# Optimization experiments

Measured on AMD Instinct MI355X. Metric: run time of the kernel, lower is better.

The kernel has to match this reference:

```python
import jax, jax.numpy as jnp
import numpy as np

N_NODES = 50000
N_EDGES = 800000
NODE_DIM = 256
EDGE_DIM = 64
HIDDEN = 256
LN_EPS = 1e-5


def setup_inputs() -> dict:
    key = jax.random.key(0)
    ks = jax.random.split(key, 12)
    s = 0.05
    return {
        "edge_attr": jax.random.normal(ks[0], (N_EDGES, EDGE_DIM), jnp.float32),
        "node_attr": jax.random.normal(ks[1], (N_NODES, NODE_DIM), jnp.float32),
        "edge_index": jax.random.randint(ks[2], (2, N_EDGES), 0, N_NODES, jnp.int64),
        # split first linear: [hidden, edge_dim], [hidden, node_dim], [hidden, node_dim]
        "edge_lin": jax.random.normal(ks[3], (HIDDEN, EDGE_DIM), jnp.float32) * s,
        "src_lin": jax.random.normal(ks[4], (HIDDEN, NODE_DIM), jnp.float32) * s,
        "dst_lin": jax.random.normal(ks[5], (HIDDEN, NODE_DIM), jnp.float32) * s,
        "bias": jax.random.normal(ks[6], (HIDDEN,), jnp.float32) * s,
        # mlp: ReLU -> Linear(hidden,hidden) -> ReLU -> Linear(hidden,edge_dim) -> LayerNorm
        "W1": jax.random.normal(ks[7], (HIDDEN, HIDDEN), jnp.float32) * s,
        "b1": jax.random.normal(ks[8], (HIDDEN,), jnp.float32) * s,
        "W2": jax.random.normal(ks[9], (EDGE_DIM, HIDDEN), jnp.float32) * s,
        "b2": jax.random.normal(ks[10], (EDGE_DIM,), jnp.float32) * s,
        "ln_gamma": jnp.ones((EDGE_DIM,), jnp.float32),
        "ln_beta": jnp.zeros((EDGE_DIM,), jnp.float32),
    }


def reference(edge_attr, node_attr, edge_index, edge_lin, src_lin, dst_lin,
              bias, W1, b1, W2, b2, ln_gamma, ln_beta):
    # pre-project nodes once, then gather per-edge (sum trick)
    mlp_edge = edge_attr @ edge_lin.T                 # [E, H]
    mlp_src = node_attr @ src_lin.T                   # [N, H]
    mlp_dst = node_attr @ dst_lin.T + bias            # [N, H]
    src, dst = edge_index[0], edge_index[1]
    h = mlp_edge + mlp_src[src] + mlp_dst[dst]        # [E, H]
    # MLP: ReLU -> Linear -> ReLU -> Linear -> LayerNorm
    h = jax.nn.relu(h)
    h = jax.nn.relu(h @ W1.T + b1)                    # [E, H]
    y = h @ W2.T + b2                                 # [E, edge_dim]
    mu = jnp.mean(y, axis=-1, keepdims=True)
    var = jnp.mean(jnp.square(y - mu), axis=-1, keepdims=True)
    y = (y - mu) * jax.lax.rsqrt(var + LN_EPS) * ln_gamma + ln_beta
    return y
```

## Files before the change

kernel.cpp:

```cpp
#include <hip/hip_runtime.h>
#include <stdint.h>

#define EN 800000
#define NN 50000
#define HID 256
#define ED 64
#define LN_EPS 1e-5f

typedef __attribute__((ext_vector_type(8))) short bf8_t;
typedef __attribute__((ext_vector_type(4))) float f32x4;

union BF8 { unsigned short u[8]; bf8_t v; };

__device__ __forceinline__ unsigned short f2bf(float f) {
  union { float f; uint32_t u; } x; x.f = f;
  return (unsigned short)((x.u + 0x7FFFu + ((x.u >> 16) & 1u)) >> 16);
}
__device__ __forceinline__ float bf2f(uint32_t h) {
  union { uint32_t u; float f; } x; x.u = h << 16;
  return x.f;
}
__device__ __forceinline__ bf8_t pack8(float4 f0, float4 f1) {
  BF8 u;
  u.u[0] = f2bf(f0.x); u.u[1] = f2bf(f0.y); u.u[2] = f2bf(f0.z); u.u[3] = f2bf(f0.w);
  u.u[4] = f2bf(f1.x); u.u[5] = f2bf(f1.y); u.u[6] = f2bf(f1.z); u.u[7] = f2bf(f1.w);
  return u.v;
}

#define MFMA(a, b, c) __builtin_amdgcn_mfma_f32_16x16x32_bf16((a), (b), (c), 0, 0, 0)

__device__ __forceinline__ void gl_lds16(const void* g, void* l) {
  __builtin_amdgcn_global_load_lds(
      (const __attribute__((address_space(1))) void*)g,
      (__attribute__((address_space(3))) void*)l, 16, 0, 0);
}

__global__ void k_cvt_w(const float* __restrict__ W1, const float* __restrict__ W2,
                        const float* __restrict__ EL,
                        unsigned short* __restrict__ W1b, unsigned short* __restrict__ W2b,
                        unsigned short* __restrict__ ELb) {
  int i = blockIdx.x * blockDim.x + threadIdx.x;
  int stride = blockDim.x * gridDim.x;
  for (int j = i; j < HID * HID; j += stride) W1b[j] = f2bf(W1[j]);
  for (int j = i; j < ED * HID; j += stride) W2b[j] = f2bf(W2[j]);
  for (int j = i; j < HID * ED; j += stride) ELb[j] = f2bf(EL[j]);
}

__launch_bounds__(256)
__global__ void k_node_proj(const float* __restrict__ node_attr,
                            const float* __restrict__ src_lin,
                            const float* __restrict__ dst_lin,
                            const float* __restrict__ bias,
                            unsigned short* __restrict__ Psrc,
                            unsigned short* __restrict__ Pdst) {
  __shared__ __align__(16) char s_a[64 * 512];
  const int tid = threadIdx.x;
  const int wid = tid >> 6;
  const int lane = tid & 63;
  const int l16 = lane & 15, lq = lane >> 4;
  const int m0 = blockIdx.x * 64;

  for (int c = tid; c < 64 * 32; c += 256) {
    int row = c >> 5, kc = c & 31;
    int grow = m0 + row;
    bf8_t val;
    if (grow < NN) {
      const float4* p = (const float4*)(node_attr + (size_t)grow * HID + kc * 8);
      val = pack8(p[0], p[1]);
    } else {
      BF8 z;
      #pragma unroll
      for (int j = 0; j < 8; ++j) z.u[j] = 0;
      val = z.v;
    }
    *(bf8_t*)(s_a + row * 512 + ((kc ^ (row & 7)) << 4)) = val;
  }
  __syncthreads();

  const int n0 = wid * 64;
  for (int pass = 0; pass < 2; ++pass) {
    const float* W = pass ? dst_lin : src_lin;
    f32x4 acc[4][4] = {};
    #pragma unroll
    for (int ks = 0; ks < 8; ++ks) {
      bf8_t a[4], b[4];
      #pragma unroll
      for (int mi = 0; mi < 4; ++mi) {
        int row = mi * 16 + l16;
        a[mi] = *(const bf8_t*)(s_a + row * 512 + (((ks * 4 + lq) ^ (row & 7)) << 4));
      }
      #pragma unroll
      for (int ni = 0; ni < 4; ++ni) {
        const float4* p = (const float4*)(W + (size_t)(n0 + ni * 16 + l16) * HID + ks * 32 + lq * 8);
        b[ni] = pack8(p[0], p[1]);
      }
      #pragma unroll
      for (int mi = 0; mi < 4; ++mi)
        #pragma unroll
        for (int ni = 0; ni < 4; ++ni)
          acc[mi][ni] = MFMA(a[mi], b[ni], acc[mi][ni]);
    }
    unsigned short* P = pass ? Pdst : Psrc;
    #pragma unroll
    for (int ni = 0; ni < 4; ++ni) {
      int col = n0 + ni * 16 + l16;
      float bia = pass ? bias[col] : 0.f;
      #pragma unroll
      for (int mi = 0; mi < 4; ++mi) {
        #pragma unroll
        for (int r = 0; r < 4; ++r) {
          int row = m0 + mi * 16 + lq * 4 + r;
          if (row < NN) P[(size_t)row * HID + col] = f2bf(acc[mi][ni][r] + bia);
        }
      }
    }
  }
}

__launch_bounds__(256, 3)
__global__ void k_gather_g1(const float* __restrict__ edge_attr,
                            const int* __restrict__ edge_index,
                            const unsigned short* __restrict__ Psrc,
                            const unsigned short* __restrict__ Pdst,
                            const unsigned short* __restrict__ ELb,
                            unsigned short* __restrict__ H0,
                            int chunk_base) {
  __shared__ __align__(16) char s_h[64 * 512];
  __shared__ __align__(16) char s_e[64 * 128];
  __shared__ int s_src[64], s_dst[64];

  const int tid = threadIdx.x;
  const int wid = tid >> 6;
  const int lane = tid & 63;
  const int l16 = lane & 15, lq = lane >> 4;
  const int e0 = chunk_base + blockIdx.x * 64;
  const int h0 = blockIdx.x * 64;
  const int n0 = wid * 64;

  if (tid < 64) s_src[tid] = edge_index[e0 + tid];
  else if (tid < 128) s_dst[tid - 64] = edge_index[EN + e0 + (tid - 64)];

  #pragma unroll
  for (int i = 0; i < 2; ++i) {
    int c = tid + i * 256;
    int row = c >> 3, kc = c & 7;
    const float4* p = (const float4*)(edge_attr + (size_t)(e0 + row) * ED + kc * 8);
    *(bf8_t*)(s_e + row * 128 + ((kc ^ (row & 7)) << 4)) = pack8(p[0], p[1]);
  }
  __syncthreads();

  #pragma unroll 4
  for (int i = 0; i < 16; ++i) {
    int er = wid * 16 + i;
    int s = s_src[er], d = s_dst[er];
    const uint2* ps = (const uint2*)(Psrc + (size_t)s * HID) + lane;
    const uint2* pd = (const uint2*)(Pdst + (size_t)d * HID) + lane;
    uint2 a = *ps, b = *pd;
    float v0 = bf2f(a.x & 0xffffu) + bf2f(b.x & 0xffffu);
    float v1 = bf2f(a.x >> 16)     + bf2f(b.x >> 16);
    float v2 = bf2f(a.y & 0xffffu) + bf2f(b.y & 0xffffu);
    float v3 = bf2f(a.y >> 16)     + bf2f(b.y >> 16);
    uint2 o;
    o.x = (uint32_t)f2bf(v0) | ((uint32_t)f2bf(v1) << 16);
    o.y = (uint32_t)f2bf(v2) | ((uint32_t)f2bf(v3) << 16);
    int chunk = lane >> 1;
    *(uint2*)(s_h + er * 512 + ((chunk ^ (er & 7)) << 4) + ((lane & 1) << 3)) = o;
  }

  f32x4 acc[4][4] = {};
  #pragma unroll
  for (int ks = 0; ks < 2; ++ks) {
    bf8_t a[4], b[4];
    #pragma unroll
    for (int mi = 0; mi < 4; ++mi) {
      int row = mi * 16 + l16;
      a[mi] = *(const bf8_t*)(s_e + row * 128 + (((ks * 4 + lq) ^ (row & 7)) << 4));
    }
    #pragma unroll
    for (int ni = 0; ni < 4; ++ni)
      b[ni] = *(const bf8_t*)(ELb + (n0 + ni * 16 + l16) * ED + ks * 32 + lq * 8);
    #pragma unroll
    for (int mi = 0; mi < 4; ++mi)
      #pragma unroll
      for (int ni = 0; ni < 4; ++ni)
        acc[mi][ni] = MFMA(a[mi], b[ni], acc[mi][ni]);
  }
  __syncthreads();

  #pragma unroll
  for (int mi = 0; mi < 4; ++mi) {
    #pragma unroll
    for (int ni = 0; ni < 4; ++ni) {
      int col = n0 + ni * 16 + l16;
      #pragma unroll
      for (int r = 0; r < 4; ++r) {
        int row = mi * 16 + lq * 4 + r;
        unsigned short* p = (unsigned short*)(s_h + row * 512 +
                              (((col >> 3) ^ (row & 7)) << 4) + ((col & 7) << 1));
        float v = acc[mi][ni][r] + bf2f(*p);
        *p = f2bf(fmaxf(v, 0.f));
      }
    }
  }
  __syncthreads();

  #pragma unroll
  for (int i = 0; i < 8; ++i) {
    int c = tid + i * 256;
    int row = c >> 5, kc = c & 31;
    bf8_t val = *(const bf8_t*)(s_h + row * 512 + ((kc ^ (row & 7)) << 4));
    *(bf8_t*)(H0 + ((size_t)(h0 + row) << 8) + kc * 8) = val;
  }
}

__launch_bounds__(256, 2)
__global__ void k_mlp(const unsigned short* __restrict__ H0,
                      const unsigned short* __restrict__ W1b,
                      const unsigned short* __restrict__ W2b,
                      const float* __restrict__ b1,
                      const float* __restrict__ b2,
                      const float* __restrict__ gam,
                      const float* __restrict__ bet,
                      float* __restrict__ out,
                      int chunk_base) {
  __shared__ __align__(16) char s_a[64 * 512];
  __shared__ __align__(16) char s_b[256 * 128];

  const int tid = threadIdx.x;
  const int wid = tid >> 6;
  const int lane = tid & 63;
  const int l16 = lane & 15, lq = lane >> 4;
  const int eloc = blockIdx.x * 64;
  const int eglob = chunk_base + eloc;
  const int n0 = wid * 64;

  #pragma unroll
  for (int i = 0; i < 8; ++i) {
    int c = wid * 8 + i;
    int row = 2 * c + (lane >> 5);
    int srcc = (lane & 31) ^ (row & 7);
    gl_lds16(H0 + ((size_t)(eloc + row) << 8) + srcc * 8, s_a + c * 1024);
  }

  f32x4 acc[4][4] = {};
  for (int ks = 0; ks < 4; ++ks) {
    if (ks) __syncthreads();
    #pragma unroll
    for (int i = 0; i < 8; ++i) {
      int c = wid * 8 + i;
      int rown = 8 * c + (lane >> 3);
      int srcc = (lane & 7) ^ (rown & 7);
      gl_lds16(W1b + (size_t)rown * HID + ks * 64 + srcc * 8, s_b + c * 1024);
    }
    __syncthreads();

    #pragma unroll
    for (int ks2 = 0; ks2 < 2; ++ks2) {
      bf8_t a[4], b[4];
      #pragma unroll
      for (int mi = 0; mi < 4; ++mi) {
        int row = mi * 16 + l16;
        int c16 = ks * 8 + ks2 * 4 + lq;
        a[mi] = *(const bf8_t*)(s_a + row * 512 + ((c16 ^ (row & 7)) << 4));
      }
      #pragma unroll
      for (int ni = 0; ni < 4; ++ni) {
        int row = n0 + ni * 16 + l16;
        int c16 = ks2 * 4 + lq;
        b[ni] = *(const bf8_t*)(s_b + row * 128 + ((c16 ^ (row & 7)) << 4));
      }
      #pragma unroll
      for (int mi = 0; mi < 4; ++mi)
        #pragma unroll
        for (int ni = 0; ni < 4; ++ni)
          acc[mi][ni] = MFMA(a[mi], b[ni], acc[mi][ni]);
    }
  }
  __syncthreads();

  #pragma unroll
  for (int ni = 0; ni < 4; ++ni) {
    int col = n0 + ni * 16 + l16;
    float bia = b1[col];
    #pragma unroll
    for (int mi = 0; mi < 4; ++mi) {
      #pragma unroll
      for (int r = 0; r < 4; ++r) {
        int row = mi * 16 + lq * 4 + r;
        *(unsigned short*)(s_a + row * 512 +
            (((col >> 3) ^ (row & 7)) << 4) + ((col & 7) << 1))
            = f2bf(fmaxf(acc[mi][ni][r] + bia, 0.f));
      }
    }
  }
  __syncthreads();

  f32x4 acc3[4] = {};
  #pragma unroll
  for (int ks = 0; ks < 8; ++ks) {
    int row = wid * 16 + l16;
    bf8_t a = *(const bf8_t*)(s_a + row * 512 + (((ks * 4 + lq) ^ (row & 7)) << 4));
    #pragma unroll
    for (int ni = 0; ni < 4; ++ni) {
      bf8_t b = *(const bf8_t*)(W2b + (ni * 16 + l16) * HID + ks * 32 + lq * 8);
      acc3[ni] = MFMA(a, b, acc3[ni]);
    }
  }

  float vals[4][4];
  float sum[4] = {0.f, 0.f, 0.f, 0.f}, ssq[4] = {0.f, 0.f, 0.f, 0.f};
  #pragma unroll
  for (int ni = 0; ni < 4; ++ni) {
    int col = ni * 16 + l16;
    float bia = b2[col];
    #pragma unroll
    for (int r = 0; r < 4; ++r) {
      float v = acc3[ni][r] + bia;
      vals[ni][r] = v;
      sum[r] += v;
      ssq[r] += v * v;
    }
  }
  #pragma unroll
  for (int m = 1; m < 16; m <<= 1) {
    #pragma unroll
    for (int r = 0; r < 4; ++r) {
      sum[r] += __shfl_xor(sum[r], m, 64);
      ssq[r] += __shfl_xor(ssq[r], m, 64);
    }
  }
  float mu[4], rstd[4];
  #pragma unroll
  for (int r = 0; r < 4; ++r) {
    mu[r] = sum[r] * (1.f / 64.f);
    float var = ssq[r] * (1.f / 64.f) - mu[r] * mu[r];
    rstd[r] = rsqrtf(var + LN_EPS);
  }
  #pragma unroll
  for (int ni = 0; ni < 4; ++ni) {
    int col = ni * 16 + l16;
    float g = gam[col], be = bet[col];
    #pragma unroll
    for (int r = 0; r < 4; ++r) {
      int row = eglob + wid * 16 + lq * 4 + r;
      out[(size_t)row * ED + col] = (vals[ni][r] - mu[r]) * rstd[r] * g + be;
    }
  }
}

__launch_bounds__(256)
__global__ void k_edge_fused(const float* __restrict__ edge_attr,
                             const int* __restrict__ edge_index,
                             const unsigned short* __restrict__ Psrc,
                             const unsigned short* __restrict__ Pdst,
                             const unsigned short* __restrict__ ELb,
                             const unsigned short* __restrict__ W1b,
                             const unsigned short* __restrict__ W2b,
                             const float* __restrict__ b1,
                             const float* __restrict__ b2,
                             const float* __restrict__ gam,
                             const float* __restrict__ bet,
                             float* __restrict__ out) {
  __shared__ __align__(16) char s_h[64 * 512];
  __shared__ __align__(16) char s_e[64 * 128];
  __shared__ int s_src[64], s_dst[64];

  const int tid = threadIdx.x;
  const int wid = tid >> 6;
  const int lane = tid & 63;
  const int l16 = lane & 15, lq = lane >> 4;
  const int e0 = blockIdx.x * 64;

  if (tid < 64) s_src[tid] = edge_index[e0 + tid];
  else if (tid < 128) s_dst[tid - 64] = edge_index[EN + e0 + (tid - 64)];

  #pragma unroll
  for (int i = 0; i < 2; ++i) {
    int c = tid + i * 256;
    int row = c >> 3, kc = c & 7;
    const float4* p = (const float4*)(edge_attr + (size_t)(e0 + row) * ED + kc * 8);
    *(bf8_t*)(s_e + row * 128 + ((kc ^ (row & 7)) << 4)) = pack8(p[0], p[1]);
  }
  __syncthreads();

  #pragma unroll 4
  for (int i = 0; i < 16; ++i) {
    int er = wid * 16 + i;
    int s = s_src[er], d = s_dst[er];
    const uint2* ps = (const uint2*)(Psrc + (size_t)s * HID) + lane;
    const uint2* pd = (const uint2*)(Pdst + (size_t)d * HID) + lane;
    uint2 a = *ps, b = *pd;
    float v0 = bf2f(a.x & 0xffffu) + bf2f(b.x & 0xffffu);
    float v1 = bf2f(a.x >> 16)     + bf2f(b.x >> 16);
    float v2 = bf2f(a.y & 0xffffu) + bf2f(b.y & 0xffffu);
    float v3 = bf2f(a.y >> 16)     + bf2f(b.y >> 16);
    uint2 o;
    o.x = (uint32_t)f2bf(v0) | ((uint32_t)f2bf(v1) << 16);
    o.y = (uint32_t)f2bf(v2) | ((uint32_t)f2bf(v3) << 16);
    int chunk = lane >> 1;
    *(uint2*)(s_h + er * 512 + ((chunk ^ (er & 7)) << 4) + ((lane & 1) << 3)) = o;
  }

  const int n0 = wid * 64;
  f32x4 acc[4][4] = {};
  #pragma unroll
  for (int ks = 0; ks < 2; ++ks) {
    bf8_t a[4], b[4];
    #pragma unroll
    for (int mi = 0; mi < 4; ++mi) {
      int row = mi * 16 + l16;
      a[mi] = *(const bf8_t*)(s_e + row * 128 + (((ks * 4 + lq) ^ (row & 7)) << 4));
    }
    #pragma unroll
    for (int ni = 0; ni < 4; ++ni)
      b[ni] = *(const bf8_t*)(ELb + (n0 + ni * 16 + l16) * ED + ks * 32 + lq * 8);
    #pragma unroll
    for (int mi = 0; mi < 4; ++mi)
      #pragma unroll
      for (int ni = 0; ni < 4; ++ni)
        acc[mi][ni] = MFMA(a[mi], b[ni], acc[mi][ni]);
  }
  __syncthreads();

  #pragma unroll
  for (int mi = 0; mi < 4; ++mi) {
    #pragma unroll
    for (int ni = 0; ni < 4; ++ni) {
      int col = n0 + ni * 16 + l16;
      #pragma unroll
      for (int r = 0; r < 4; ++r) {
        int row = mi * 16 + lq * 4 + r;
        unsigned short* p = (unsigned short*)(s_h + row * 512 +
                              (((col >> 3) ^ (row & 7)) << 4) + ((col & 7) << 1));
        float v = acc[mi][ni][r] + bf2f(*p);
        *p = f2bf(fmaxf(v, 0.f));
      }
    }
  }
  __syncthreads();

  #pragma unroll
  for (int mi = 0; mi < 4; ++mi)
    #pragma unroll
    for (int ni = 0; ni < 4; ++ni)
      acc[mi][ni] = (f32x4){0.f, 0.f, 0.f, 0.f};
  #pragma unroll
  for (int ks = 0; ks < 8; ++ks) {
    bf8_t a[4], b[4];
    #pragma unroll
    for (int mi = 0; mi < 4; ++mi) {
      int row = mi * 16 + l16;
      a[mi] = *(const bf8_t*)(s_h + row * 512 + (((ks * 4 + lq) ^ (row & 7)) << 4));
    }
    #pragma unroll
    for (int ni = 0; ni < 4; ++ni)
      b[ni] = *(const bf8_t*)(W1b + (size_t)(n0 + ni * 16 + l16) * HID + ks * 32 + lq * 8);
    #pragma unroll
    for (int mi = 0; mi < 4; ++mi)
      #pragma unroll
      for (int ni = 0; ni < 4; ++ni)
        acc[mi][ni] = MFMA(a[mi], b[ni], acc[mi][ni]);
  }
  __syncthreads();

  #pragma unroll
  for (int ni = 0; ni < 4; ++ni) {
    int col = n0 + ni * 16 + l16;
    float bia = b1[col];
    #pragma unroll
    for (int mi = 0; mi < 4; ++mi) {
      #pragma unroll
      for (int r = 0; r < 4; ++r) {
        int row = mi * 16 + lq * 4 + r;
        *(unsigned short*)(s_h + row * 512 +
            (((col >> 3) ^ (row & 7)) << 4) + ((col & 7) << 1))
            = f2bf(fmaxf(acc[mi][ni][r] + bia, 0.f));
      }
    }
  }
  __syncthreads();

  f32x4 acc3[4] = {};
  #pragma unroll
  for (int ks = 0; ks < 8; ++ks) {
    int row = wid * 16 + l16;
    bf8_t a = *(const bf8_t*)(s_h + row * 512 + (((ks * 4 + lq) ^ (row & 7)) << 4));
    #pragma unroll
    for (int ni = 0; ni < 4; ++ni) {
      bf8_t b = *(const bf8_t*)(W2b + (ni * 16 + l16) * HID + ks * 32 + lq * 8);
      acc3[ni] = MFMA(a, b, acc3[ni]);
    }
  }

  float vals[4][4];
  float sum[4] = {0.f, 0.f, 0.f, 0.f}, ssq[4] = {0.f, 0.f, 0.f, 0.f};
  #pragma unroll
  for (int ni = 0; ni < 4; ++ni) {
    int col = ni * 16 + l16;
    float bia = b2[col];
    #pragma unroll
    for (int r = 0; r < 4; ++r) {
      float v = acc3[ni][r] + bia;
      vals[ni][r] = v;
      sum[r] += v;
      ssq[r] += v * v;
    }
  }
  #pragma unroll
  for (int m = 1; m < 16; m <<= 1) {
    #pragma unroll
    for (int r = 0; r < 4; ++r) {
      sum[r] += __shfl_xor(sum[r], m, 64);
      ssq[r] += __shfl_xor(ssq[r], m, 64);
    }
  }
  float mu[4], rstd[4];
  #pragma unroll
  for (int r = 0; r < 4; ++r) {
    mu[r] = sum[r] * (1.f / 64.f);
    float var = ssq[r] * (1.f / 64.f) - mu[r] * mu[r];
    rstd[r] = rsqrtf(var + LN_EPS);
  }
  #pragma unroll
  for (int ni = 0; ni < 4; ++ni) {
    int col = ni * 16 + l16;
    float g = gam[col], be = bet[col];
    #pragma unroll
    for (int r = 0; r < 4; ++r) {
      int row = e0 + wid * 16 + lq * 4 + r;
      out[(size_t)row * ED + col] = (vals[ni][r] - mu[r]) * rstd[r] * g + be;
    }
  }
}

#define TAB_END 51396608ull

extern "C" void kernel_launch(void* const* d_in, const int* in_sizes, int n_in,
                              void* d_out, int out_size, void* d_ws, size_t ws_size,
                              hipStream_t stream) {
  const float* edge_attr = (const float*)d_in[0];
  const float* node_attr = (const float*)d_in[1];
  const int* edge_index = (const int*)d_in[2];
  const float* edge_lin = (const float*)d_in[3];
  const float* src_lin = (const float*)d_in[4];
  const float* dst_lin = (const float*)d_in[5];
  const float* bias = (const float*)d_in[6];
  const float* W1 = (const float*)d_in[7];
  const float* b1 = (const float*)d_in[8];
  const float* W2 = (const float*)d_in[9];
  const float* b2 = (const float*)d_in[10];
  const float* gam = (const float*)d_in[11];
  const float* bet = (const float*)d_in[12];
  float* out = (float*)d_out;

  char* ws = (char*)d_ws;
  unsigned short* Psrc = (unsigned short*)(ws + 0);
  unsigned short* Pdst = (unsigned short*)(ws + 25600000);
  unsigned short* W1b  = (unsigned short*)(ws + 51200000);
  unsigned short* W2b  = (unsigned short*)(ws + 51331072);
  unsigned short* ELb  = (unsigned short*)(ws + 51363840);
  unsigned short* H0   = (unsigned short*)(ws + TAB_END);

  hipLaunchKernelGGL(k_cvt_w, dim3(128), dim3(256), 0, stream,
                     W1, W2, edge_lin, W1b, W2b, ELb);
  hipLaunchKernelGGL(k_node_proj, dim3((NN + 63) / 64), dim3(256), 0, stream,
                     node_attr, src_lin, dst_lin, bias, Psrc, Pdst);

  long long avail = (ws_size > TAB_END) ? (long long)(ws_size - TAB_END) : 0;
  long long chunk = (avail / 512) / 64 * 64;
  if (chunk > EN) chunk = EN;

  if (chunk >= 64) {
    for (long long base = 0; base < EN; base += chunk) {
      long long cnt = EN - base < chunk ? EN - base : chunk;
      int cblk = (int)(cnt / 64);
      hipLaunchKernelGGL(k_gather_g1, dim3(cblk), dim3(256), 0, stream,
                         edge_attr, edge_index, Psrc, Pdst, ELb, H0, (int)base);
      hipLaunchKernelGGL(k_mlp, dim3(cblk), dim3(256), 0, stream,
                         H0, W1b, W2b, b1, b2, gam, bet, out, (int)base);
    }
  } else {
    hipLaunchKernelGGL(k_edge_fused, dim3(EN / 64), dim3(256), 0, stream,
                       edge_attr, edge_index, Psrc, Pdst, ELb, W1b, W2b,
                       b1, b2, gam, bet, out);
  }
}
```

Baseline: 753.3 us.

## Batch gather loads, shrink W1 LDS tile for occupancy, cap chunk size

```diff
diff --git a/kernel.cpp b/kernel.cpp
--- a/kernel.cpp
+++ b/kernel.cpp
@@ -6,6 +6,7 @@
 #define HID 256
 #define ED 64
 #define LN_EPS 1e-5f
+#define CHUNK_MAX 131072LL
 
 typedef __attribute__((ext_vector_type(8))) short bf8_t;
 typedef __attribute__((ext_vector_type(4))) float f32x4;
@@ -149,22 +150,28 @@
   }
   __syncthreads();
 
-  #pragma unroll 4
-  for (int i = 0; i < 16; ++i) {
-    int er = wid * 16 + i;
-    int s = s_src[er], d = s_dst[er];
-    const uint2* ps = (const uint2*)(Psrc + (size_t)s * HID) + lane;
-    const uint2* pd = (const uint2*)(Pdst + (size_t)d * HID) + lane;
-    uint2 a = *ps, b = *pd;
-    float v0 = bf2f(a.x & 0xffffu) + bf2f(b.x & 0xffffu);
-    float v1 = bf2f(a.x >> 16)     + bf2f(b.x >> 16);
-    float v2 = bf2f(a.y & 0xffffu) + bf2f(b.y & 0xffffu);
-    float v3 = bf2f(a.y >> 16)     + bf2f(b.y >> 16);
-    uint2 o;
-    o.x = (uint32_t)f2bf(v0) | ((uint32_t)f2bf(v1) << 16);
-    o.y = (uint32_t)f2bf(v2) | ((uint32_t)f2bf(v3) << 16);
-    int chunk = lane >> 1;
-    *(uint2*)(s_h + er * 512 + ((chunk ^ (er & 7)) << 4) + ((lane & 1) << 3)) = o;
+  #pragma unroll
+  for (int half = 0; half < 2; ++half) {
+    uint2 pa[8], pb[8];
+    #pragma unroll
+    for (int i = 0; i < 8; ++i) {
+      int er = wid * 16 + half * 8 + i;
+      pa[i] = *((const uint2*)(Psrc + (size_t)s_src[er] * HID) + lane);
+      pb[i] = *((const uint2*)(Pdst + (size_t)s_dst[er] * HID) + lane);
+    }
+    #pragma unroll
+    for (int i = 0; i < 8; ++i) {
+      int er = wid * 16 + half * 8 + i;
+      float v0 = bf2f(pa[i].x & 0xffffu) + bf2f(pb[i].x & 0xffffu);
+      float v1 = bf2f(pa[i].x >> 16)     + bf2f(pb[i].x >> 16);
+      float v2 = bf2f(pa[i].y & 0xffffu) + bf2f(pb[i].y & 0xffffu);
+      float v3 = bf2f(pa[i].y >> 16)     + bf2f(pb[i].y >> 16);
+      uint2 o;
+      o.x = (uint32_t)f2bf(v0) | ((uint32_t)f2bf(v1) << 16);
+      o.y = (uint32_t)f2bf(v2) | ((uint32_t)f2bf(v3) << 16);
+      int chunk = lane >> 1;
+      *(uint2*)(s_h + er * 512 + ((chunk ^ (er & 7)) << 4) + ((lane & 1) << 3)) = o;
+    }
   }
 
   f32x4 acc[4][4] = {};
@@ -213,7 +220,7 @@
   }
 }
 
-__launch_bounds__(256, 2)
+__launch_bounds__(256, 3)
 __global__ void k_mlp(const unsigned short* __restrict__ H0,
                       const unsigned short* __restrict__ W1b,
                       const unsigned short* __restrict__ W2b,
@@ -224,7 +231,7 @@
                       float* __restrict__ out,
                       int chunk_base) {
   __shared__ __align__(16) char s_a[64 * 512];
-  __shared__ __align__(16) char s_b[256 * 128];
+  __shared__ __align__(16) char s_b[256 * 64];
 
   const int tid = threadIdx.x;
   const int wid = tid >> 6;
@@ -243,38 +250,35 @@
   }
 
   f32x4 acc[4][4] = {};
-  for (int ks = 0; ks < 4; ++ks) {
+  for (int ks = 0; ks < 8; ++ks) {
     if (ks) __syncthreads();
     #pragma unroll
-    for (int i = 0; i < 8; ++i) {
-      int c = wid * 8 + i;
-      int rown = 8 * c + (lane >> 3);
-      int srcc = (lane & 7) ^ (rown & 7);
-      gl_lds16(W1b + (size_t)rown * HID + ks * 64 + srcc * 8, s_b + c * 1024);
+    for (int i = 0; i < 4; ++i) {
+      int c = wid * 4 + i;
+      int rown = c * 16 + (lane >> 2);
+      int srcc = (lane & 3) ^ (rown & 3) ^ ((rown >> 2) & 3);
+      gl_lds16(W1b + (size_t)rown * HID + ks * 32 + srcc * 8, s_b + c * 1024);
     }
     __syncthreads();
 
-    #pragma unroll
-    for (int ks2 = 0; ks2 < 2; ++ks2) {
-      bf8_t a[4], b[4];
-      #pragma unroll
-      for (int mi = 0; mi < 4; ++mi) {
-        int row = mi * 16 + l16;
-        int c16 = ks * 8 + ks2 * 4 + lq;
-        a[mi] = *(const bf8_t*)(s_a + row * 512 + ((c16 ^ (row & 7)) << 4));
-      }
-      #pragma unroll
-      for (int ni = 0; ni < 4; ++ni) {
-        int row = n0 + ni * 16 + l16;
-        int c16 = ks2 * 4 + lq;
-        b[ni] = *(const bf8_t*)(s_b + row * 128 + ((c16 ^ (row & 7)) << 4));
-      }
-      #pragma unroll
-      for (int mi = 0; mi < 4; ++mi)
-        #pragma unroll
-        for (int ni = 0; ni < 4; ++ni)
-          acc[mi][ni] = MFMA(a[mi], b[ni], acc[mi][ni]);
-    }
+    bf8_t a[4], b[4];
+    #pragma unroll
+    for (int mi = 0; mi < 4; ++mi) {
+      int row = mi * 16 + l16;
+      int c16 = ks * 4 + lq;
+      a[mi] = *(const bf8_t*)(s_a + row * 512 + ((c16 ^ (row & 7)) << 4));
+    }
+    #pragma unroll
+    for (int ni = 0; ni < 4; ++ni) {
+      int row = n0 + ni * 16 + l16;
+      int sl = lq ^ (row & 3) ^ ((row >> 2) & 3);
+      b[ni] = *(const bf8_t*)(s_b + row * 64 + (sl << 4));
+    }
+    #pragma unroll
+    for (int mi = 0; mi < 4; ++mi)
+      #pragma unroll
+      for (int ni = 0; ni < 4; ++ni)
+        acc[mi][ni] = MFMA(a[mi], b[ni], acc[mi][ni]);
   }
   __syncthreads();
 
@@ -568,6 +572,7 @@
 
   long long avail = (ws_size > TAB_END) ? (long long)(ws_size - TAB_END) : 0;
   long long chunk = (avail / 512) / 64 * 64;
+  if (chunk > CHUNK_MAX) chunk = CHUNK_MAX;
   if (chunk > EN) chunk = EN;
 
   if (chunk >= 64) {
```

New measurement: 786.3 us. 4.4% more time.
